# Performance work log

Measured on AMD Instinct MI355X. Metric: run time of the kernel, lower is better.

The kernel has to match this reference:

```python
import jax, jax.numpy as jnp
import numpy as np

N_NODES = 100000
N_EDGES = 1600000
VOCAB = 50000
F_DIM = 128
N_GRAPHS = 64
N_LABELS = 20


def setup_inputs() -> dict:
    key = jax.random.key(0)
    ks = jax.random.split(key, 12)
    s = 1.0 / np.sqrt(F_DIM)
    inp = {
        "x": jax.random.randint(ks[0], (N_NODES,), 0, VOCAB),
        "edge_index": jax.random.randint(ks[1], (2, N_EDGES), 0, N_NODES),
        "batch": jnp.sort(jax.random.randint(ks[2], (N_NODES,), 0, N_GRAPHS)),
        "emb": jax.random.normal(ks[3], (VOCAB, F_DIM), jnp.float32),
        "w1_rel": jax.random.normal(ks[4], (F_DIM, F_DIM), jnp.float32) * s,
        "w1_root": jax.random.normal(ks[5], (F_DIM, F_DIM), jnp.float32) * s,
        "b1": jnp.zeros((F_DIM,), jnp.float32),
        "w2_rel": jax.random.normal(ks[6], (F_DIM, F_DIM), jnp.float32) * s,
        "w2_root": jax.random.normal(ks[7], (F_DIM, F_DIM), jnp.float32) * s,
        "b2": jnp.zeros((F_DIM,), jnp.float32),
        "lw1": jax.random.normal(ks[8], (2 * F_DIM, 128), jnp.float32) * (1.0 / np.sqrt(2 * F_DIM)),
        "lb1": jnp.zeros((128,), jnp.float32),
        "lw2": jax.random.normal(ks[9], (128, 64), jnp.float32) * (1.0 / np.sqrt(128)),
        "lb2": jnp.zeros((64,), jnp.float32),
        "lw3": jax.random.normal(ks[10], (64, N_LABELS), jnp.float32) * (1.0 / np.sqrt(64)),
        "lb3": jnp.zeros((N_LABELS,), jnp.float32),
    }
    return inp


def graph_conv(h, src, dst, w_rel, w_root, b):
    # PyG GraphConv (aggr='add'): out_i = W_rel @ sum_{j->i} h_j + b + W_root @ h_i
    agg = jax.ops.segment_sum(h[src], dst, num_segments=N_NODES)  # [N, F]
    return agg @ w_rel + b + h @ w_root


def reference(x, edge_index, batch, emb, w1_rel, w1_root, b1,
              w2_rel, w2_root, b2, lw1, lb1, lw2, lb2, lw3, lb3):
    src, dst = edge_index[0], edge_index[1]
    h = emb[x]                                              # [N, F]
    h = jax.nn.relu(graph_conv(h, src, dst, w1_rel, w1_root, b1))
    h = jax.nn.relu(graph_conv(h, src, dst, w2_rel, w2_root, b2))
    # global max pool + global mean pool per graph
    gmax = jax.ops.segment_max(h, batch, num_segments=N_GRAPHS)  # [G, F]
    gsum = jax.ops.segment_sum(h, batch, num_segments=N_GRAPHS)
    counts = jax.ops.segment_sum(jnp.ones((N_NODES,), h.dtype), batch,
                                 num_segments=N_GRAPHS)
    gmean = gsum / jnp.maximum(counts, 1.0)[:, None]
    g = jnp.concatenate([gmax, gmean], axis=1)              # [G, 2F]
    g = jax.nn.relu(g @ lw1 + lb1)
    g = jax.nn.relu(g @ lw2 + lb2)
    # NOTE: original applies log_softmax over dim=0 (the graph dim) - kept faithful
    return jax.nn.log_softmax(g @ lw3 + lb3, axis=0)
```

## Files before the change

### kernel.cpp

```cpp
#include <hip/hip_runtime.h>
#include <hip/hip_bf16.h>

#define N_NODES   100000
#define N_EDGES   1600000
#define N_GRAPHS  64
#define FDIM      128
#define N_LABELS  20
#define NBK       64
#define P_BKT     1563
#define NCHUNKS   512
#define NCHUNKS_LOG 9
#define CHUNK     3125
#define SCAN_M    (P_BKT * NCHUNKS)
#define SB1_BLOCKS 3126
#define SB_BLOCKS 391
#define BPITCH    136
#define PCHUNKS   32

typedef __bf16 bf16x8 __attribute__((ext_vector_type(8)));
typedef float  f32x4  __attribute__((ext_vector_type(4)));
union frag_u { uint4 u; bf16x8 b; };

__device__ __forceinline__ unsigned bfr(float v) {
  unsigned b = __float_as_uint(v);
  return (b + 0x7fffu + ((b >> 16) & 1u)) >> 16;
}

__global__ __launch_bounds__(256) void init_kernel(
    float* __restrict__ pool, float* __restrict__ zrow,
    int* __restrict__ csr, int* __restrict__ csr2, int* __restrict__ offsets) {
  int i = blockIdx.x * 256 + threadIdx.x;
  if (i < N_GRAPHS * 256) pool[i] = 0.f;
  if (i < FDIM) zrow[i] = 0.f;
  if (i < 16) { csr[N_EDGES + i] = 0; csr2[N_EDGES + i] = 0; }
  if (i == 16) offsets[N_NODES] = N_EDGES;
}

__global__ __launch_bounds__(256) void cvt_emb_kernel(
    const float* __restrict__ emb, unsigned short* __restrict__ embbf) {
  int i = blockIdx.x * 256 + threadIdx.x;
  float4 v = ((const float4*)emb)[i];
  uint2 o;
  o.x = bfr(v.x) | (bfr(v.y) << 16);
  o.y = bfr(v.z) | (bfr(v.w) << 16);
  ((uint2*)embbf)[i] = o;
}

__global__ __launch_bounds__(256) void cvt_w_kernel(
    const float* __restrict__ w1rel, const float* __restrict__ w1rt,
    const float* __restrict__ w2rel, const float* __restrict__ w2rt,
    unsigned short* __restrict__ wt1, unsigned short* __restrict__ wt2) {
  int gid = blockIdx.x * 256 + threadIdx.x;
  int l = gid >> 15;
  int rem = gid & 32767;
  int c = rem >> 8, k = rem & 255;
  const float* w = l ? ((k < 128) ? w2rel : w2rt) : ((k < 128) ? w1rel : w1rt);
  float v = w[(size_t)(k & 127) * FDIM + c];
  (l ? wt2 : wt1)[c * 256 + k] = (unsigned short)bfr(v);
}

__global__ __launch_bounds__(256) void histA_kernel(
    const int* __restrict__ ei, int* __restrict__ cntmat) {
  __shared__ int hist[P_BKT];
  int tid = threadIdx.x;
  for (int i = tid; i < P_BKT; i += 256) hist[i] = 0;
  __syncthreads();
  int base = blockIdx.x * CHUNK;
  for (int i = tid; i < CHUNK; i += 256) {
    int d = ei[N_EDGES + base + i];
    atomicAdd(&hist[d >> 6], 1);
  }
  __syncthreads();
  for (int p = tid; p < P_BKT; p += 256)
    cntmat[p * NCHUNKS + blockIdx.x] = hist[p];
}

__global__ __launch_bounds__(256) void scanB1_kernel(
    const int* __restrict__ v, int* __restrict__ part,
    int* __restrict__ bsum) {
  __shared__ int s[256];
  int tid = threadIdx.x;
  int i = blockIdx.x * 256 + tid;
  int val = (i < SCAN_M) ? v[i] : 0;
  s[tid] = val;
  __syncthreads();
  for (int off = 1; off < 256; off <<= 1) {
    int t = (tid >= off) ? s[tid - off] : 0;
    __syncthreads();
    s[tid] += t;
    __syncthreads();
  }
  if (i < SCAN_M) part[i] = s[tid] - val;
  if (tid == 255) bsum[blockIdx.x] = s[255];
}

__global__ __launch_bounds__(512) void scanB2_kernel(int* __restrict__ bsum) {
  __shared__ int s[512];
  int tid = threadIdx.x;
  int v[8];
  int tot = 0;
#pragma unroll
  for (int j = 0; j < 8; ++j) {
    int idx = tid * 8 + j;
    v[j] = (idx < SB1_BLOCKS) ? bsum[idx] : 0;
    tot += v[j];
  }
  s[tid] = tot;
  __syncthreads();
  for (int off = 1; off < 512; off <<= 1) {
    int t = (tid >= off) ? s[tid - off] : 0;
    __syncthreads();
    s[tid] += t;
    __syncthreads();
  }
  int run = s[tid] - tot;
#pragma unroll
  for (int j = 0; j < 8; ++j) {
    int idx = tid * 8 + j;
    int val = v[j];
    if (idx < SB1_BLOCKS) bsum[idx] = run;
    run += val;
  }
}

__global__ __launch_bounds__(256) void scanB3_kernel(
    int* __restrict__ part, const int* __restrict__ bsum,
    int* __restrict__ bstart) {
  int i = blockIdx.x * 256 + threadIdx.x;
  if (i < SCAN_M) {
    int o = part[i] + bsum[blockIdx.x];
    part[i] = o;
    if ((i & (NCHUNKS - 1)) == 0) bstart[i >> NCHUNKS_LOG] = o;
  }
  if (blockIdx.x == 0 && threadIdx.x == 0) bstart[P_BKT] = N_EDGES;
}

__global__ __launch_bounds__(256) void scatA_kernel(
    const int* __restrict__ ei, const int* __restrict__ S,
    int* __restrict__ ebuf) {
  __shared__ int rc[P_BKT];
  int tid = threadIdx.x;
  for (int p = tid; p < P_BKT; p += 256)
    rc[p] = S[p * NCHUNKS + blockIdx.x];
  __syncthreads();
  int base = blockIdx.x * CHUNK;
  for (int i = tid; i < CHUNK; i += 256) {
    int s0 = ei[base + i];
    int d0 = ei[N_EDGES + base + i];
    int pos = atomicAdd(&rc[d0 >> 6], 1);
    ebuf[pos] = (s0 << 6) | (d0 & 63);
  }
}

__global__ __launch_bounds__(256) void fill2_kernel(
    const int* __restrict__ ebuf, const int* __restrict__ bstart,
    const int* __restrict__ x, int* __restrict__ offsets,
    int* __restrict__ csr, int* __restrict__ csr2) {
  __shared__ int ldeg[NBK], loffs[NBK], rc2[NBK];
  int tid = threadIdx.x;
  int p = blockIdx.x;
  int beg = bstart[p], end = bstart[p + 1];
  if (tid < NBK) ldeg[tid] = 0;
  __syncthreads();
  for (int i = beg + tid; i < end; i += 256)
    atomicAdd(&ldeg[ebuf[i] & 63], 1);
  __syncthreads();
  if (tid == 0) {
    int run = 0;
    for (int r = 0; r < NBK; ++r) { loffs[r] = run; run += ldeg[r]; }
  }
  __syncthreads();
  if (tid < NBK) {
    rc2[tid] = loffs[tid];
    int gn = p * NBK + tid;
    if (gn < N_NODES) offsets[gn] = beg + loffs[tid];
  }
  __syncthreads();
  for (int i = beg + tid; i < end; i += 256) {
    int e = ebuf[i];
    int ld = e & 63;
    int src = e >> 6;
    int pos = atomicAdd(&rc2[ld], 1);
    csr[beg + pos] = src;
    csr2[beg + pos] = x[src];
  }
}

__global__ __launch_bounds__(256) void agg_kernel(
    const unsigned short* __restrict__ feat, const int* __restrict__ srcidx,
    const int* __restrict__ offs, const float* __restrict__ zrow,
    unsigned short* __restrict__ aggout) {
  int sub = threadIdx.x >> 4;
  int fq  = threadIdx.x & 15;
  int node = blockIdx.x * 16 + sub;

  float4 e0 = make_float4(0.f, 0.f, 0.f, 0.f);
  float4 e1 = make_float4(0.f, 0.f, 0.f, 0.f);
  float4 o0 = make_float4(0.f, 0.f, 0.f, 0.f);
  float4 o1 = make_float4(0.f, 0.f, 0.f, 0.f);
  int s = offs[node], e = offs[node + 1];

  const uint4* __restrict__ fb = (const uint4*)feat;
  const uint4* __restrict__ zb = (const uint4*)zrow;

  int p = s;
  for (; p + 8 <= e; p += 8) {
    const uint4* rp[8];
#pragma unroll
    for (int u = 0; u < 8; ++u)
      rp[u] = fb + (size_t)srcidx[p + u] * 16;
    uint4 w[8];
#pragma unroll
    for (int u = 0; u < 8; ++u) w[u] = rp[u][fq];
#pragma unroll
    for (int u = 0; u < 8; ++u) {
      float4& A = (u & 1) ? o0 : e0;
      float4& B = (u & 1) ? o1 : e1;
      A.x += __uint_as_float(w[u].x << 16);
      A.y += __uint_as_float(w[u].x & 0xffff0000u);
      A.z += __uint_as_float(w[u].y << 16);
      A.w += __uint_as_float(w[u].y & 0xffff0000u);
      B.x += __uint_as_float(w[u].z << 16);
      B.y += __uint_as_float(w[u].z & 0xffff0000u);
      B.z += __uint_as_float(w[u].w << 16);
      B.w += __uint_as_float(w[u].w & 0xffff0000u);
    }
  }
  if (p < e) {
    const uint4* rp[8];
#pragma unroll
    for (int u = 0; u < 8; ++u) {
      int iu = srcidx[p + u];
      rp[u] = (p + u < e) ? (fb + (size_t)iu * 16) : zb;
    }
    uint4 w[8];
#pragma unroll
    for (int u = 0; u < 8; ++u) w[u] = rp[u][fq];
#pragma unroll
    for (int u = 0; u < 8; ++u) {
      float4& A = (u & 1) ? o0 : e0;
      float4& B = (u & 1) ? o1 : e1;
      A.x += __uint_as_float(w[u].x << 16);
      A.y += __uint_as_float(w[u].x & 0xffff0000u);
      A.z += __uint_as_float(w[u].y << 16);
      A.w += __uint_as_float(w[u].y & 0xffff0000u);
      B.x += __uint_as_float(w[u].z << 16);
      B.y += __uint_as_float(w[u].z & 0xffff0000u);
      B.z += __uint_as_float(w[u].w << 16);
      B.w += __uint_as_float(w[u].w & 0xffff0000u);
    }
  }
  float f0 = e0.x + o0.x, f1 = e0.y + o0.y, f2 = e0.z + o0.z, f3 = e0.w + o0.w;
  float f4 = e1.x + o1.x, f5 = e1.y + o1.y, f6 = e1.z + o1.z, f7 = e1.w + o1.w;
  uint4 o;
  o.x = bfr(f0) | (bfr(f1) << 16);
  o.y = bfr(f2) | (bfr(f3) << 16);
  o.z = bfr(f4) | (bfr(f5) << 16);
  o.w = bfr(f6) | (bfr(f7) << 16);
  ((uint4*)aggout)[(size_t)node * 16 + fq] = o;
}

__global__ __launch_bounds__(256, 2) void gemm_kernel(
    const unsigned short* __restrict__ aggbf,
    const unsigned short* __restrict__ rootbf,
    const int* __restrict__ hidx,
    const unsigned short* __restrict__ wt,
    const float* __restrict__ bias,
    float* __restrict__ hout_f32,
    unsigned short* __restrict__ hout_bf) {
  __shared__ unsigned short B_s[128 * BPITCH];
  int tid = threadIdx.x;
  int nodeBase = blockIdx.x * 128;
  int lane = tid & 63;
  int wv = tid >> 6;
  int wbase = wv * 32;
  int lo = lane & 15, hi = lane >> 4;

  int gnode[2], hroot[2];
#pragma unroll
  for (int mt = 0; mt < 2; ++mt) {
    int g = nodeBase + wbase + mt * 16 + lo;
    if (g > N_NODES - 1) g = N_NODES - 1;
    gnode[mt] = g;
    hroot[mt] = hidx ? hidx[g] : g;
  }

  frag_u afr[2][8];
#pragma unroll
  for (int mt = 0; mt < 2; ++mt) {
#pragma unroll
    for (int t = 0; t < 4; ++t)
      afr[mt][t].u =
          *(const uint4*)(aggbf + (size_t)gnode[mt] * FDIM + t * 32 + hi * 8);
#pragma unroll
    for (int t = 0; t < 4; ++t)
      afr[mt][4 + t].u =
          *(const uint4*)(rootbf + (size_t)hroot[mt] * FDIM + t * 32 + hi * 8);
  }

  f32x4 acc[2][8];
#pragma unroll
  for (int nt = 0; nt < 8; ++nt) {
    float b = bias[nt * 16 + lo];
#pragma unroll
    for (int mt = 0; mt < 2; ++mt) {
      acc[mt][nt][0] = b; acc[mt][nt][1] = b;
      acc[mt][nt][2] = b; acc[mt][nt][3] = b;
    }
  }

  int sr = tid >> 1;
  int so = (tid & 1) * 64;

#pragma unroll
  for (int h = 0; h < 2; ++h) {
    __syncthreads();
#pragma unroll
    for (int i = 0; i < 8; ++i)
      *(uint4*)(B_s + sr * BPITCH + so + i * 8) =
          *(const uint4*)(wt + sr * 256 + h * 128 + so + i * 8);
    __syncthreads();
#pragma unroll
    for (int tt = 0; tt < 4; ++tt) {
      frag_u bfv[8];
#pragma unroll
      for (int nt = 0; nt < 8; ++nt)
        bfv[nt].u =
            *(const uint4*)&B_s[(nt * 16 + lo) * BPITCH + tt * 32 + hi * 8];
#pragma unroll
      for (int mt = 0; mt < 2; ++mt)
#pragma unroll
        for (int nt = 0; nt < 8; ++nt)
          acc[mt][nt] = __builtin_amdgcn_mfma_f32_16x16x32_bf16(
              afr[mt][h * 4 + tt].b, bfv[nt].b, acc[mt][nt], 0, 0, 0);
    }
  }

#pragma unroll
  for (int mt = 0; mt < 2; ++mt) {
#pragma unroll
    for (int r = 0; r < 4; ++r) {
      int n = nodeBase + wbase + mt * 16 + hi * 4 + r;
      if (n < N_NODES) {
        if (hout_bf) {
          unsigned short* o = hout_bf + (size_t)n * FDIM + lo;
#pragma unroll
          for (int nt = 0; nt < 8; ++nt)
            o[nt * 16] = (unsigned short)bfr(fmaxf(acc[mt][nt][r], 0.f));
        } else {
          float* o = hout_f32 + (size_t)n * FDIM + lo;
#pragma unroll
          for (int nt = 0; nt < 8; ++nt)
            o[nt * 16] = fmaxf(acc[mt][nt][r], 0.f);
        }
      }
    }
  }
}

__global__ void find_starts_kernel(const int* __restrict__ batch,
                                   int* __restrict__ start) {
  int i = blockIdx.x * 256 + threadIdx.x;
  if (i >= N_NODES) return;
  int b  = batch[i];
  int bp = (i == 0) ? -1 : batch[i - 1];
  for (int g = bp + 1; g <= b; ++g) start[g] = i;
  if (i == N_NODES - 1) {
    for (int g = b + 1; g <= N_GRAPHS; ++g) start[g] = N_NODES;
  }
}

__global__ __launch_bounds__(256) void pool_kernel(
    const float* __restrict__ h2, const int* __restrict__ start,
    float* __restrict__ pool) {
  __shared__ float4 rmax[8][32];
  __shared__ float4 rsum[8][32];
  int g = blockIdx.x >> 5;
  int c = blockIdx.x & (PCHUNKS - 1);
  int tid = threadIdx.x;
  int fq = tid & 31;
  int sub = tid >> 5;
  int s = start[g], e = start[g + 1];
  int len = e - s;
  int lo = s + (int)(((long long)len * c) >> 5);
  int hi = s + (int)(((long long)len * (c + 1)) >> 5);
  float4 mx = make_float4(0.f, 0.f, 0.f, 0.f);
  float4 sm = make_float4(0.f, 0.f, 0.f, 0.f);
  for (int n = lo + sub; n < hi; n += 8) {
    float4 v = ((const float4*)(h2 + (size_t)n * FDIM))[fq];
    mx.x = fmaxf(mx.x, v.x); mx.y = fmaxf(mx.y, v.y);
    mx.z = fmaxf(mx.z, v.z); mx.w = fmaxf(mx.w, v.w);
    sm.x += v.x; sm.y += v.y; sm.z += v.z; sm.w += v.w;
  }
  rmax[sub][fq] = mx;
  rsum[sub][fq] = sm;
  __syncthreads();
  if (sub == 0) {
#pragma unroll
    for (int r = 1; r < 8; ++r) {
      float4 m2 = rmax[r][fq], s2 = rsum[r][fq];
      mx.x = fmaxf(mx.x, m2.x); mx.y = fmaxf(mx.y, m2.y);
      mx.z = fmaxf(mx.z, m2.z); mx.w = fmaxf(mx.w, m2.w);
      sm.x += s2.x; sm.y += s2.y; sm.z += s2.z; sm.w += s2.w;
    }
    unsigned int* pm = (unsigned int*)&pool[g * 256 + fq * 4];
    atomicMax(pm + 0, __float_as_uint(mx.x));
    atomicMax(pm + 1, __float_as_uint(mx.y));
    atomicMax(pm + 2, __float_as_uint(mx.z));
    atomicMax(pm + 3, __float_as_uint(mx.w));
    float* ps = &pool[g * 256 + 128 + fq * 4];
    atomicAdd(ps + 0, sm.x);
    atomicAdd(ps + 1, sm.y);
    atomicAdd(ps + 2, sm.z);
    atomicAdd(ps + 3, sm.w);
  }
}

__global__ void pool_fin_kernel(float* __restrict__ pool,
                                const int* __restrict__ start) {
  int gid = blockIdx.x * 256 + threadIdx.x;
  int g = gid >> 7, f = gid & 127;
  int cnt = start[g + 1] - start[g];
  float c = (float)(cnt > 1 ? cnt : 1);
  pool[g * 256 + 128 + f] /= c;
}

__global__ void head1_kernel(const float* __restrict__ pool,
                             const float* __restrict__ lw1,
                             const float* __restrict__ lb1,
                             float* __restrict__ t1) {
  int gid = blockIdx.x * 256 + threadIdx.x;
  int r = gid >> 7, c = gid & 127;
  float acc = lb1[c];
  for (int k = 0; k < 256; ++k) acc += pool[r * 256 + k] * lw1[k * 128 + c];
  t1[gid] = fmaxf(acc, 0.f);
}

__global__ void head2_kernel(const float* __restrict__ t1,
                             const float* __restrict__ lw2,
                             const float* __restrict__ lb2,
                             float* __restrict__ t2) {
  int gid = blockIdx.x * 256 + threadIdx.x;
  int r = gid >> 6, c = gid & 63;
  float acc = lb2[c];
  for (int k = 0; k < 128; ++k) acc += t1[r * 128 + k] * lw2[k * 64 + c];
  t2[gid] = fmaxf(acc, 0.f);
}

__global__ __launch_bounds__(256) void head3_kernel(
    const float* __restrict__ t2, const float* __restrict__ lw3,
    const float* __restrict__ lb3, float* __restrict__ out) {
  __shared__ float lg[N_GRAPHS * N_LABELS];
  __shared__ float col[N_LABELS];
  int tid = threadIdx.x;
  for (int o = tid; o < N_GRAPHS * N_LABELS; o += 256) {
    int r = o / N_LABELS, c = o - r * N_LABELS;
    float acc = lb3[c];
    for (int k = 0; k < 64; ++k) acc += t2[r * 64 + k] * lw3[k * N_LABELS + c];
    lg[o] = acc;
  }
  __syncthreads();
  if (tid < N_LABELS) {
    float m = -1e30f;
    for (int r = 0; r < N_GRAPHS; ++r) m = fmaxf(m, lg[r * N_LABELS + tid]);
    float s = 0.f;
    for (int r = 0; r < N_GRAPHS; ++r) s += expf(lg[r * N_LABELS + tid] - m);
    col[tid] = m + logf(s);
  }
  __syncthreads();
  for (int o = tid; o < N_GRAPHS * N_LABELS; o += 256) {
    int c = o % N_LABELS;
    out[o] = lg[o] - col[c];
  }
}

extern "C" void kernel_launch(void* const* d_in, const int* in_sizes, int n_in,
                              void* d_out, int out_size, void* d_ws, size_t ws_size,
                              hipStream_t stream) {
  const int*   x     = (const int*)  d_in[0];
  const int*   ei    = (const int*)  d_in[1];
  const int*   batch = (const int*)  d_in[2];
  const float* emb   = (const float*)d_in[3];
  const float* w1rel = (const float*)d_in[4];
  const float* w1rt  = (const float*)d_in[5];
  const float* b1    = (const float*)d_in[6];
  const float* w2rel = (const float*)d_in[7];
  const float* w2rt  = (const float*)d_in[8];
  const float* b2    = (const float*)d_in[9];
  const float* lw1   = (const float*)d_in[10];
  const float* lb1   = (const float*)d_in[11];
  const float* lw2   = (const float*)d_in[12];
  const float* lb2   = (const float*)d_in[13];
  const float* lw3   = (const float*)d_in[14];
  const float* lb3   = (const float*)d_in[15];
  float* out = (float*)d_out;

  char* ws = (char*)d_ws;
  const size_t HB   = 51200000;
  const size_t CSRB = 6400128;
  const size_t OFFB = 400128;
  float* hB      = (float*)(ws);
  unsigned short* embbf = (unsigned short*)(ws);
  int*   cntmat  = (int*)  (ws + 13000000);
  int*   S       = (int*)  (ws + 16500000);
  int*   bsum    = (int*)  (ws + 20000000);
  unsigned short* aggbf = (unsigned short*)(ws + HB);
  int*   ebuf    = (int*)  (ws + HB);
  int*   csr     = (int*)  (ws + 2 * HB);
  int*   csr2    = (int*)  (ws + 2 * HB + CSRB);
  int*   offsets = (int*)  (ws + 2 * HB + 2 * CSRB);
  int*   bstart  = (int*)  (ws + 2 * HB + 2 * CSRB + OFFB);
  float* zrow    = (float*)(ws + 2 * HB + 2 * CSRB + OFFB + 6400);
  int*   start   = (int*)  (ws + 2 * HB + 2 * CSRB + OFFB + 6912);
  float* pool    = (float*)(ws + 2 * HB + 2 * CSRB + OFFB + 7424);
  float* t1      = (float*)(ws + 2 * HB + 2 * CSRB + OFFB + 72960);
  float* t2      = (float*)(ws + 2 * HB + 2 * CSRB + OFFB + 105728);
  unsigned short* hbf =
      (unsigned short*)(ws + 2 * HB + 2 * CSRB + OFFB + 122112);
  unsigned short* wt1 =
      (unsigned short*)(ws + 2 * HB + 2 * CSRB + OFFB + 122112 + 25600000);
  unsigned short* wt2 = wt1 + 128 * 256;

  init_kernel<<<64, 256, 0, stream>>>(pool, zrow, csr, csr2, offsets);

  cvt_emb_kernel<<<6250, 256, 0, stream>>>(emb, embbf);
  cvt_w_kernel<<<256, 256, 0, stream>>>(w1rel, w1rt, w2rel, w2rt, wt1, wt2);

  histA_kernel<<<NCHUNKS, 256, 0, stream>>>(ei, cntmat);
  scanB1_kernel<<<SB1_BLOCKS, 256, 0, stream>>>(cntmat, S, bsum);
  scanB2_kernel<<<1, 512, 0, stream>>>(bsum);
  scanB3_kernel<<<SB1_BLOCKS, 256, 0, stream>>>(S, bsum, bstart);
  scatA_kernel<<<NCHUNKS, 256, 0, stream>>>(ei, S, ebuf);
  fill2_kernel<<<P_BKT, 256, 0, stream>>>(ebuf, bstart, x, offsets, csr, csr2);

  agg_kernel<<<N_NODES / 16, 256, 0, stream>>>(embbf, csr2, offsets, zrow, aggbf);
  gemm_kernel<<<(N_NODES + 127) / 128, 256, 0, stream>>>(
      aggbf, embbf, x, wt1, b1, (float*)nullptr, hbf);

  agg_kernel<<<N_NODES / 16, 256, 0, stream>>>(hbf, csr, offsets, zrow, aggbf);
  gemm_kernel<<<(N_NODES + 127) / 128, 256, 0, stream>>>(
      aggbf, hbf, (const int*)nullptr, wt2, b2, hB,
      (unsigned short*)nullptr);

  find_starts_kernel<<<SB_BLOCKS, 256, 0, stream>>>(batch, start);
  pool_kernel<<<N_GRAPHS * PCHUNKS, 256, 0, stream>>>(hB, start, pool);
  pool_fin_kernel<<<32, 256, 0, stream>>>(pool, start);

  head1_kernel<<<32, 256, 0, stream>>>(pool, lw1, lb1, t1);
  head2_kernel<<<16, 256, 0, stream>>>(t1, lw2, lb2, t2);
  head3_kernel<<<1, 256, 0, stream>>>(t2, lw3, lb3, out);
}
```

Baseline: 380.4 us.

## Software-pipeline edge gathers in aggregation and merge prep kernels into one launch

The aggregation kernel now double-buffers its neighbour index and feature loads, issuing the next batch of eight gathers before accumulating the current batch so memory latency overlaps with the adds. Separately, init, embedding conversion, weight conversion and graph-start finding are merged into one block-partitioned prep kernel to save launches. The pipelined loop reads indices up to 16 entries past a node's end, so the zero padding after the CSR arrays was widened from 16 to 32. It also holds more registers for the two buffers, which may lower occupancy.

```diff
diff --git a/kernel.cpp b/kernel.cpp
--- a/kernel.cpp
+++ b/kernel.cpp
@@ -26,37 +26,48 @@
   return (b + 0x7fffu + ((b >> 16) & 1u)) >> 16;
 }
 
-__global__ __launch_bounds__(256) void init_kernel(
-    float* __restrict__ pool, float* __restrict__ zrow,
-    int* __restrict__ csr, int* __restrict__ csr2, int* __restrict__ offsets) {
-  int i = blockIdx.x * 256 + threadIdx.x;
-  if (i < N_GRAPHS * 256) pool[i] = 0.f;
-  if (i < FDIM) zrow[i] = 0.f;
-  if (i < 16) { csr[N_EDGES + i] = 0; csr2[N_EDGES + i] = 0; }
-  if (i == 16) offsets[N_NODES] = N_EDGES;
-}
-
-__global__ __launch_bounds__(256) void cvt_emb_kernel(
-    const float* __restrict__ emb, unsigned short* __restrict__ embbf) {
-  int i = blockIdx.x * 256 + threadIdx.x;
-  float4 v = ((const float4*)emb)[i];
-  uint2 o;
-  o.x = bfr(v.x) | (bfr(v.y) << 16);
-  o.y = bfr(v.z) | (bfr(v.w) << 16);
-  ((uint2*)embbf)[i] = o;
-}
-
-__global__ __launch_bounds__(256) void cvt_w_kernel(
+__global__ __launch_bounds__(256) void prep_kernel(
+    const float* __restrict__ emb, unsigned short* __restrict__ embbf,
     const float* __restrict__ w1rel, const float* __restrict__ w1rt,
     const float* __restrict__ w2rel, const float* __restrict__ w2rt,
-    unsigned short* __restrict__ wt1, unsigned short* __restrict__ wt2) {
-  int gid = blockIdx.x * 256 + threadIdx.x;
-  int l = gid >> 15;
-  int rem = gid & 32767;
-  int c = rem >> 8, k = rem & 255;
-  const float* w = l ? ((k < 128) ? w2rel : w2rt) : ((k < 128) ? w1rel : w1rt);
-  float v = w[(size_t)(k & 127) * FDIM + c];
-  (l ? wt2 : wt1)[c * 256 + k] = (unsigned short)bfr(v);
+    unsigned short* __restrict__ wt1, unsigned short* __restrict__ wt2,
+    const int* __restrict__ batch, int* __restrict__ start,
+    float* __restrict__ pool, float* __restrict__ zrow,
+    int* __restrict__ csr, int* __restrict__ csr2,
+    int* __restrict__ offsets) {
+  int b = blockIdx.x;
+  int tid = threadIdx.x;
+  if (b < 6250) {
+    int i = b * 256 + tid;
+    float4 v = ((const float4*)emb)[i];
+    uint2 o;
+    o.x = bfr(v.x) | (bfr(v.y) << 16);
+    o.y = bfr(v.z) | (bfr(v.w) << 16);
+    ((uint2*)embbf)[i] = o;
+  } else if (b < 6506) {
+    int gid = (b - 6250) * 256 + tid;
+    int l = gid >> 15;
+    int rem = gid & 32767;
+    int c = rem >> 8, k = rem & 255;
+    const float* w = l ? ((k < 128) ? w2rel : w2rt) : ((k < 128) ? w1rel : w1rt);
+    float v = w[(size_t)(k & 127) * FDIM + c];
+    (l ? wt2 : wt1)[c * 256 + k] = (unsigned short)bfr(v);
+  } else if (b < 6897) {
+    int i = (b - 6506) * 256 + tid;
+    if (i >= N_NODES) return;
+    int bb = batch[i];
+    int bp = (i == 0) ? -1 : batch[i - 1];
+    for (int g = bp + 1; g <= bb; ++g) start[g] = i;
+    if (i == N_NODES - 1) {
+      for (int g = bb + 1; g <= N_GRAPHS; ++g) start[g] = N_NODES;
+    }
+  } else {
+    int i = (b - 6897) * 256 + tid;
+    if (i < N_GRAPHS * 256) pool[i] = 0.f;
+    if (i < FDIM) zrow[i] = 0.f;
+    if (i < 32) { csr[N_EDGES + i] = 0; csr2[N_EDGES + i] = 0; }
+    if (i == 32) offsets[N_NODES] = N_EDGES;
+  }
 }
 
 __global__ __launch_bounds__(256) void histA_kernel(
@@ -186,6 +197,32 @@
   }
 }
 
+#define LOADIDX(I, P)                                      \
+  { _Pragma("unroll")                                      \
+    for (int u = 0; u < 8; ++u) I[u] = srcidx[(P) + u]; }
+
+#define GATHERW(W, I, P)                                   \
+  { _Pragma("unroll")                                      \
+    for (int u = 0; u < 8; ++u) {                          \
+      const uint4* rp = ((P) + u < e) ? (fb + (size_t)I[u] * 16) : zb; \
+      W[u] = rp[fq];                                       \
+    } }
+
+#define ACCG(W)                                            \
+  { _Pragma("unroll")                                      \
+    for (int u = 0; u < 8; ++u) {                          \
+      float4& A = (u & 1) ? o0 : e0;                       \
+      float4& B = (u & 1) ? o1 : e1;                       \
+      A.x += __uint_as_float(W[u].x << 16);                \
+      A.y += __uint_as_float(W[u].x & 0xffff0000u);        \
+      A.z += __uint_as_float(W[u].y << 16);                \
+      A.w += __uint_as_float(W[u].y & 0xffff0000u);        \
+      B.x += __uint_as_float(W[u].z << 16);                \
+      B.y += __uint_as_float(W[u].z & 0xffff0000u);        \
+      B.z += __uint_as_float(W[u].w << 16);                \
+      B.w += __uint_as_float(W[u].w & 0xffff0000u);        \
+    } }
+
 __global__ __launch_bounds__(256) void agg_kernel(
     const unsigned short* __restrict__ feat, const int* __restrict__ srcidx,
     const int* __restrict__ offs, const float* __restrict__ zrow,
@@ -203,53 +240,28 @@
   const uint4* __restrict__ fb = (const uint4*)feat;
   const uint4* __restrict__ zb = (const uint4*)zrow;
 
+  int iA[8], iB[8];
+  uint4 wA[8], wB[8];
+
+  LOADIDX(iA, s);
+  LOADIDX(iB, s + 8);
+  GATHERW(wA, iA, s);
+
   int p = s;
-  for (; p + 8 <= e; p += 8) {
-    const uint4* rp[8];
-#pragma unroll
-    for (int u = 0; u < 8; ++u)
-      rp[u] = fb + (size_t)srcidx[p + u] * 16;
-    uint4 w[8];
-#pragma unroll
-    for (int u = 0; u < 8; ++u) w[u] = rp[u][fq];
-#pragma unroll
-    for (int u = 0; u < 8; ++u) {
-      float4& A = (u & 1) ? o0 : e0;
-      float4& B = (u & 1) ? o1 : e1;
-      A.x += __uint_as_float(w[u].x << 16);
-      A.y += __uint_as_float(w[u].x & 0xffff0000u);
-      A.z += __uint_as_float(w[u].y << 16);
-      A.w += __uint_as_float(w[u].y & 0xffff0000u);
-      B.x += __uint_as_float(w[u].z << 16);
-      B.y += __uint_as_float(w[u].z & 0xffff0000u);
-      B.z += __uint_as_float(w[u].w << 16);
-      B.w += __uint_as_float(w[u].w & 0xffff0000u);
-    }
-  }
-  if (p < e) {
-    const uint4* rp[8];
-#pragma unroll
-    for (int u = 0; u < 8; ++u) {
-      int iu = srcidx[p + u];
-      rp[u] = (p + u < e) ? (fb + (size_t)iu * 16) : zb;
-    }
-    uint4 w[8];
-#pragma unroll
-    for (int u = 0; u < 8; ++u) w[u] = rp[u][fq];
-#pragma unroll
-    for (int u = 0; u < 8; ++u) {
-      float4& A = (u & 1) ? o0 : e0;
-      float4& B = (u & 1) ? o1 : e1;
-      A.x += __uint_as_float(w[u].x << 16);
-      A.y += __uint_as_float(w[u].x & 0xffff0000u);
-      A.z += __uint_as_float(w[u].y << 16);
-      A.w += __uint_as_float(w[u].y & 0xffff0000u);
-      B.x += __uint_as_float(w[u].z << 16);
-      B.y += __uint_as_float(w[u].z & 0xffff0000u);
-      B.z += __uint_as_float(w[u].w << 16);
-      B.w += __uint_as_float(w[u].w & 0xffff0000u);
-    }
-  }
+  while (true) {
+    int pn = p + 8;
+    if (pn >= e) { ACCG(wA); break; }
+    LOADIDX(iA, pn + 8);
+    GATHERW(wB, iB, pn);
+    ACCG(wA);
+    p = pn; pn = p + 8;
+    if (pn >= e) { ACCG(wB); break; }
+    LOADIDX(iB, pn + 8);
+    GATHERW(wA, iA, pn);
+    ACCG(wB);
+    p = pn;
+  }
+
   float f0 = e0.x + o0.x, f1 = e0.y + o0.y, f2 = e0.z + o0.z, f3 = e0.w + o0.w;
   float f4 = e1.x + o1.x, f5 = e1.y + o1.y, f6 = e1.z + o1.z, f7 = e1.w + o1.w;
   uint4 o;
@@ -355,18 +367,6 @@
         }
       }
     }
-  }
-}
-
-__global__ void find_starts_kernel(const int* __restrict__ batch,
-                                   int* __restrict__ start) {
-  int i = blockIdx.x * 256 + threadIdx.x;
-  if (i >= N_NODES) return;
-  int b  = batch[i];
-  int bp = (i == 0) ? -1 : batch[i - 1];
-  for (int g = bp + 1; g <= b; ++g) start[g] = i;
-  if (i == N_NODES - 1) {
-    for (int g = b + 1; g <= N_GRAPHS; ++g) start[g] = N_NODES;
   }
 }
 
@@ -521,10 +521,9 @@
       (unsigned short*)(ws + 2 * HB + 2 * CSRB + OFFB + 122112 + 25600000);
   unsigned short* wt2 = wt1 + 128 * 256;
 
-  init_kernel<<<64, 256, 0, stream>>>(pool, zrow, csr, csr2, offsets);
-
-  cvt_emb_kernel<<<6250, 256, 0, stream>>>(emb, embbf);
-  cvt_w_kernel<<<256, 256, 0, stream>>>(w1rel, w1rt, w2rel, w2rt, wt1, wt2);
+  prep_kernel<<<6961, 256, 0, stream>>>(emb, embbf, w1rel, w1rt, w2rel, w2rt,
+                                        wt1, wt2, batch, start, pool, zrow,
+                                        csr, csr2, offsets);
 
   histA_kernel<<<NCHUNKS, 256, 0, stream>>>(ei, cntmat);
   scanB1_kernel<<<SB1_BLOCKS, 256, 0, stream>>>(cntmat, S, bsum);
@@ -542,7 +541,6 @@
       aggbf, hbf, (const int*)nullptr, wt2, b2, hB,
       (unsigned short*)nullptr);
 
-  find_starts_kernel<<<SB_BLOCKS, 256, 0, stream>>>(batch, start);
   pool_kernel<<<N_GRAPHS * PCHUNKS, 256, 0, stream>>>(hB, start, pool);
   pool_fin_kernel<<<32, 256, 0, stream>>>(pool, start);
 
```

Measured after the change: 392.7 us. 1.03x slower.

## Fuse neighbor aggregation with MFMA GEMM per layer and merge prep kernels

Applied to the files above, without the earlier changes.

Folds each layer's edge aggregation and its dense GEMM into one kernel. The aggregated and root rows for 16 nodes are staged in shared memory and multiplied right away with MFMA, using weight fragments read straight from global memory. This removes the bf16 aggregation buffer's write and re-read and two launches per layer. In exchange, each block reloads the full 64KB weight matrix from global/L2 for only 16 nodes, with little reuse per block. It also merges the init, embedding/weight conversion and graph-start kernels into one prep launch to cut launch overhead.

```diff
diff --git a/kernel.cpp b/kernel.cpp
--- a/kernel.cpp
+++ b/kernel.cpp
@@ -14,8 +14,8 @@
 #define SCAN_M    (P_BKT * NCHUNKS)
 #define SB1_BLOCKS 3126
 #define SB_BLOCKS 391
-#define BPITCH    136
 #define PCHUNKS   32
+#define APAD      17
 
 typedef __bf16 bf16x8 __attribute__((ext_vector_type(8)));
 typedef float  f32x4  __attribute__((ext_vector_type(4)));
@@ -26,37 +26,48 @@
   return (b + 0x7fffu + ((b >> 16) & 1u)) >> 16;
 }
 
-__global__ __launch_bounds__(256) void init_kernel(
-    float* __restrict__ pool, float* __restrict__ zrow,
-    int* __restrict__ csr, int* __restrict__ csr2, int* __restrict__ offsets) {
-  int i = blockIdx.x * 256 + threadIdx.x;
-  if (i < N_GRAPHS * 256) pool[i] = 0.f;
-  if (i < FDIM) zrow[i] = 0.f;
-  if (i < 16) { csr[N_EDGES + i] = 0; csr2[N_EDGES + i] = 0; }
-  if (i == 16) offsets[N_NODES] = N_EDGES;
-}
-
-__global__ __launch_bounds__(256) void cvt_emb_kernel(
-    const float* __restrict__ emb, unsigned short* __restrict__ embbf) {
-  int i = blockIdx.x * 256 + threadIdx.x;
-  float4 v = ((const float4*)emb)[i];
-  uint2 o;
-  o.x = bfr(v.x) | (bfr(v.y) << 16);
-  o.y = bfr(v.z) | (bfr(v.w) << 16);
-  ((uint2*)embbf)[i] = o;
-}
-
-__global__ __launch_bounds__(256) void cvt_w_kernel(
+__global__ __launch_bounds__(256) void prep_kernel(
+    const float* __restrict__ emb, unsigned short* __restrict__ embbf,
     const float* __restrict__ w1rel, const float* __restrict__ w1rt,
     const float* __restrict__ w2rel, const float* __restrict__ w2rt,
-    unsigned short* __restrict__ wt1, unsigned short* __restrict__ wt2) {
-  int gid = blockIdx.x * 256 + threadIdx.x;
-  int l = gid >> 15;
-  int rem = gid & 32767;
-  int c = rem >> 8, k = rem & 255;
-  const float* w = l ? ((k < 128) ? w2rel : w2rt) : ((k < 128) ? w1rel : w1rt);
-  float v = w[(size_t)(k & 127) * FDIM + c];
-  (l ? wt2 : wt1)[c * 256 + k] = (unsigned short)bfr(v);
+    unsigned short* __restrict__ wt1, unsigned short* __restrict__ wt2,
+    const int* __restrict__ batch, int* __restrict__ start,
+    float* __restrict__ pool, float* __restrict__ zrow,
+    int* __restrict__ csr, int* __restrict__ csr2,
+    int* __restrict__ offsets) {
+  int b = blockIdx.x;
+  int tid = threadIdx.x;
+  if (b < 6250) {
+    int i = b * 256 + tid;
+    float4 v = ((const float4*)emb)[i];
+    uint2 o;
+    o.x = bfr(v.x) | (bfr(v.y) << 16);
+    o.y = bfr(v.z) | (bfr(v.w) << 16);
+    ((uint2*)embbf)[i] = o;
+  } else if (b < 6506) {
+    int gid = (b - 6250) * 256 + tid;
+    int l = gid >> 15;
+    int rem = gid & 32767;
+    int c = rem >> 8, k = rem & 255;
+    const float* w = l ? ((k < 128) ? w2rel : w2rt) : ((k < 128) ? w1rel : w1rt);
+    float v = w[(size_t)(k & 127) * FDIM + c];
+    (l ? wt2 : wt1)[c * 256 + k] = (unsigned short)bfr(v);
+  } else if (b < 6897) {
+    int i = (b - 6506) * 256 + tid;
+    if (i >= N_NODES) return;
+    int bb = batch[i];
+    int bp = (i == 0) ? -1 : batch[i - 1];
+    for (int g = bp + 1; g <= bb; ++g) start[g] = i;
+    if (i == N_NODES - 1) {
+      for (int g = bb + 1; g <= N_GRAPHS; ++g) start[g] = N_NODES;
+    }
+  } else {
+    int i = (b - 6897) * 256 + tid;
+    if (i < N_GRAPHS * 256) pool[i] = 0.f;
+    if (i < FDIM) zrow[i] = 0.f;
+    if (i < 32) { csr[N_EDGES + i] = 0; csr2[N_EDGES + i] = 0; }
+    if (i == 32) offsets[N_NODES] = N_EDGES;
+  }
 }
 
 __global__ __launch_bounds__(256) void histA_kernel(
@@ -186,13 +197,23 @@
   }
 }
 
-__global__ __launch_bounds__(256) void agg_kernel(
+__global__ __launch_bounds__(256) void layer_kernel(
     const unsigned short* __restrict__ feat, const int* __restrict__ srcidx,
     const int* __restrict__ offs, const float* __restrict__ zrow,
-    unsigned short* __restrict__ aggout) {
-  int sub = threadIdx.x >> 4;
-  int fq  = threadIdx.x & 15;
+    const unsigned short* __restrict__ rootbf, const int* __restrict__ hidx,
+    const unsigned short* __restrict__ wt,
+    const float* __restrict__ bias,
+    float* __restrict__ hout_f32,
+    unsigned short* __restrict__ hout_bf) {
+  __shared__ uint4 A_s[16 * APAD];
+  __shared__ uint4 R_s[16 * APAD];
+  int tid = threadIdx.x;
+  int sub = tid >> 4;
+  int fq  = tid & 15;
   int node = blockIdx.x * 16 + sub;
+
+  int hr = hidx ? hidx[node] : node;
+  uint4 rootw = ((const uint4*)rootbf)[(size_t)hr * 16 + fq];
 
   float4 e0 = make_float4(0.f, 0.f, 0.f, 0.f);
   float4 e1 = make_float4(0.f, 0.f, 0.f, 0.f);
@@ -257,116 +278,47 @@
   o.y = bfr(f2) | (bfr(f3) << 16);
   o.z = bfr(f4) | (bfr(f5) << 16);
   o.w = bfr(f6) | (bfr(f7) << 16);
-  ((uint4*)aggout)[(size_t)node * 16 + fq] = o;
-}
-
-__global__ __launch_bounds__(256, 2) void gemm_kernel(
-    const unsigned short* __restrict__ aggbf,
-    const unsigned short* __restrict__ rootbf,
-    const int* __restrict__ hidx,
-    const unsigned short* __restrict__ wt,
-    const float* __restrict__ bias,
-    float* __restrict__ hout_f32,
-    unsigned short* __restrict__ hout_bf) {
-  __shared__ unsigned short B_s[128 * BPITCH];
-  int tid = threadIdx.x;
-  int nodeBase = blockIdx.x * 128;
+  A_s[sub * APAD + fq] = o;
+  R_s[sub * APAD + fq] = rootw;
+  __syncthreads();
+
   int lane = tid & 63;
   int wv = tid >> 6;
-  int wbase = wv * 32;
   int lo = lane & 15, hi = lane >> 4;
 
-  int gnode[2], hroot[2];
-#pragma unroll
-  for (int mt = 0; mt < 2; ++mt) {
-    int g = nodeBase + wbase + mt * 16 + lo;
-    if (g > N_NODES - 1) g = N_NODES - 1;
-    gnode[mt] = g;
-    hroot[mt] = hidx ? hidx[g] : g;
-  }
-
-  frag_u afr[2][8];
-#pragma unroll
-  for (int mt = 0; mt < 2; ++mt) {
-#pragma unroll
-    for (int t = 0; t < 4; ++t)
-      afr[mt][t].u =
-          *(const uint4*)(aggbf + (size_t)gnode[mt] * FDIM + t * 32 + hi * 8);
-#pragma unroll
-    for (int t = 0; t < 4; ++t)
-      afr[mt][4 + t].u =
-          *(const uint4*)(rootbf + (size_t)hroot[mt] * FDIM + t * 32 + hi * 8);
-  }
-
-  f32x4 acc[2][8];
-#pragma unroll
-  for (int nt = 0; nt < 8; ++nt) {
-    float b = bias[nt * 16 + lo];
-#pragma unroll
-    for (int mt = 0; mt < 2; ++mt) {
-      acc[mt][nt][0] = b; acc[mt][nt][1] = b;
-      acc[mt][nt][2] = b; acc[mt][nt][3] = b;
-    }
-  }
-
-  int sr = tid >> 1;
-  int so = (tid & 1) * 64;
-
-#pragma unroll
-  for (int h = 0; h < 2; ++h) {
-    __syncthreads();
-#pragma unroll
-    for (int i = 0; i < 8; ++i)
-      *(uint4*)(B_s + sr * BPITCH + so + i * 8) =
-          *(const uint4*)(wt + sr * 256 + h * 128 + so + i * 8);
-    __syncthreads();
-#pragma unroll
-    for (int tt = 0; tt < 4; ++tt) {
-      frag_u bfv[8];
-#pragma unroll
-      for (int nt = 0; nt < 8; ++nt)
-        bfv[nt].u =
-            *(const uint4*)&B_s[(nt * 16 + lo) * BPITCH + tt * 32 + hi * 8];
-#pragma unroll
-      for (int mt = 0; mt < 2; ++mt)
-#pragma unroll
-        for (int nt = 0; nt < 8; ++nt)
-          acc[mt][nt] = __builtin_amdgcn_mfma_f32_16x16x32_bf16(
-              afr[mt][h * 4 + tt].b, bfv[nt].b, acc[mt][nt], 0, 0, 0);
-    }
-  }
-
-#pragma unroll
-  for (int mt = 0; mt < 2; ++mt) {
+  f32x4 acc[2];
+#pragma unroll
+  for (int j = 0; j < 2; ++j) {
+    float b = bias[(wv * 2 + j) * 16 + lo];
+    acc[j][0] = b; acc[j][1] = b; acc[j][2] = b; acc[j][3] = b;
+  }
+#pragma unroll
+  for (int t = 0; t < 8; ++t) {
+    frag_u a;
+    a.u = (t < 4) ? A_s[lo * APAD + t * 4 + hi]
+                  : R_s[lo * APAD + (t - 4) * 4 + hi];
+#pragma unroll
+    for (int j = 0; j < 2; ++j) {
+      int nt = wv * 2 + j;
+      frag_u bfv;
+      bfv.u = *(const uint4*)(wt + (size_t)(nt * 16 + lo) * 256 + t * 32 + hi * 8);
+      acc[j] = __builtin_amdgcn_mfma_f32_16x16x32_bf16(a.b, bfv.b, acc[j], 0, 0, 0);
+    }
+  }
+
+  int nodeBase = blockIdx.x * 16;
+#pragma unroll
+  for (int j = 0; j < 2; ++j) {
+    int nt = wv * 2 + j;
 #pragma unroll
     for (int r = 0; r < 4; ++r) {
-      int n = nodeBase + wbase + mt * 16 + hi * 4 + r;
-      if (n < N_NODES) {
-        if (hout_bf) {
-          unsigned short* o = hout_bf + (size_t)n * FDIM + lo;
-#pragma unroll
-          for (int nt = 0; nt < 8; ++nt)
-            o[nt * 16] = (unsigned short)bfr(fmaxf(acc[mt][nt][r], 0.f));
-        } else {
-          float* o = hout_f32 + (size_t)n * FDIM + lo;
-#pragma unroll
-          for (int nt = 0; nt < 8; ++nt)
-            o[nt * 16] = fmaxf(acc[mt][nt][r], 0.f);
-        }
-      }
-    }
-  }
-}
-
-__global__ void find_starts_kernel(const int* __restrict__ batch,
-                                   int* __restrict__ start) {
-  int i = blockIdx.x * 256 + threadIdx.x;
-  if (i >= N_NODES) return;
-  int b  = batch[i];
-  int bp = (i == 0) ? -1 : batch[i - 1];
-  for (int g = bp + 1; g <= b; ++g) start[g] = i;
-  if (i == N_NODES - 1) {
-    for (int g = b + 1; g <= N_GRAPHS; ++g) start[g] = N_NODES;
+      int n = nodeBase + hi * 4 + r;
+      if (hout_bf)
+        hout_bf[(size_t)n * FDIM + nt * 16 + lo] =
+            (unsigned short)bfr(fmaxf(acc[j][r], 0.f));
+      else
+        hout_f32[(size_t)n * FDIM + nt * 16 + lo] = fmaxf(acc[j][r], 0.f);
+    }
   }
 }
 
@@ -504,7 +456,6 @@
   int*   cntmat  = (int*)  (ws + 13000000);
   int*   S       = (int*)  (ws + 16500000);
   int*   bsum    = (int*)  (ws + 20000000);
-  unsigned short* aggbf = (unsigned short*)(ws + HB);
   int*   ebuf    = (int*)  (ws + HB);
   int*   csr     = (int*)  (ws + 2 * HB);
   int*   csr2    = (int*)  (ws + 2 * HB + CSRB);
@@ -521,10 +472,9 @@
       (unsigned short*)(ws + 2 * HB + 2 * CSRB + OFFB + 122112 + 25600000);
   unsigned short* wt2 = wt1 + 128 * 256;
 
-  init_kernel<<<64, 256, 0, stream>>>(pool, zrow, csr, csr2, offsets);
-
-  cvt_emb_kernel<<<6250, 256, 0, stream>>>(emb, embbf);
-  cvt_w_kernel<<<256, 256, 0, stream>>>(w1rel, w1rt, w2rel, w2rt, wt1, wt2);
+  prep_kernel<<<6961, 256, 0, stream>>>(emb, embbf, w1rel, w1rt, w2rel, w2rt,
+                                        wt1, wt2, batch, start, pool, zrow,
+                                        csr, csr2, offsets);
 
   histA_kernel<<<NCHUNKS, 256, 0, stream>>>(ei, cntmat);
   scanB1_kernel<<<SB1_BLOCKS, 256, 0, stream>>>(cntmat, S, bsum);
@@ -533,16 +483,14 @@
   scatA_kernel<<<NCHUNKS, 256, 0, stream>>>(ei, S, ebuf);
   fill2_kernel<<<P_BKT, 256, 0, stream>>>(ebuf, bstart, x, offsets, csr, csr2);
 
-  agg_kernel<<<N_NODES / 16, 256, 0, stream>>>(embbf, csr2, offsets, zrow, aggbf);
-  gemm_kernel<<<(N_NODES + 127) / 128, 256, 0, stream>>>(
-      aggbf, embbf, x, wt1, b1, (float*)nullptr, hbf);
-
-  agg_kernel<<<N_NODES / 16, 256, 0, stream>>>(hbf, csr, offsets, zrow, aggbf);
-  gemm_kernel<<<(N_NODES + 127) / 128, 256, 0, stream>>>(
-      aggbf, hbf, (const int*)nullptr, wt2, b2, hB,
-      (unsigned short*)nullptr);
-
-  find_starts_kernel<<<SB_BLOCKS, 256, 0, stream>>>(batch, start);
+  layer_kernel<<<N_NODES / 16, 256, 0, stream>>>(
+      embbf, csr2, offsets, zrow, embbf, x, wt1, b1,
+      (float*)nullptr, hbf);
+
+  layer_kernel<<<N_NODES / 16, 256, 0, stream>>>(
+      hbf, csr, offsets, zrow, hbf, (const int*)nullptr, wt2, b2,
+      hB, (unsigned short*)nullptr);
+
   pool_kernel<<<N_GRAPHS * PCHUNKS, 256, 0, stream>>>(hB, start, pool);
   pool_fin_kernel<<<32, 256, 0, stream>>>(pool, start);
 
```

Measured after the change: 417.1 us. 9.6% more time.

## Fuse graph pooling into layer-2 GEMM epilogue and merge prep kernels

Applied to the files above, without the earlier changes.

The second GEMM no longer writes the fp32 hidden matrix. It applies relu in registers and reduces max and sum per graph directly into the pool buffer with atomics, using wave shuffles when a 16-row tile belongs to one graph. This removes a 51 MB write and re-read plus the separate pool kernel. The init, embedding conversion, weight conversion and graph-start kernels are also merged into one launch to cut launch overhead. The cost is more atomics in the GEMM epilogue for tiles that span graph boundaries, and contention on 64 graph rows.

```diff
diff --git a/kernel.cpp b/kernel.cpp
--- a/kernel.cpp
+++ b/kernel.cpp
@@ -15,7 +15,6 @@
 #define SB1_BLOCKS 3126
 #define SB_BLOCKS 391
 #define BPITCH    136
-#define PCHUNKS   32
 
 typedef __bf16 bf16x8 __attribute__((ext_vector_type(8)));
 typedef float  f32x4  __attribute__((ext_vector_type(4)));
@@ -26,37 +25,48 @@
   return (b + 0x7fffu + ((b >> 16) & 1u)) >> 16;
 }
 
-__global__ __launch_bounds__(256) void init_kernel(
-    float* __restrict__ pool, float* __restrict__ zrow,
-    int* __restrict__ csr, int* __restrict__ csr2, int* __restrict__ offsets) {
-  int i = blockIdx.x * 256 + threadIdx.x;
-  if (i < N_GRAPHS * 256) pool[i] = 0.f;
-  if (i < FDIM) zrow[i] = 0.f;
-  if (i < 16) { csr[N_EDGES + i] = 0; csr2[N_EDGES + i] = 0; }
-  if (i == 16) offsets[N_NODES] = N_EDGES;
-}
-
-__global__ __launch_bounds__(256) void cvt_emb_kernel(
-    const float* __restrict__ emb, unsigned short* __restrict__ embbf) {
-  int i = blockIdx.x * 256 + threadIdx.x;
-  float4 v = ((const float4*)emb)[i];
-  uint2 o;
-  o.x = bfr(v.x) | (bfr(v.y) << 16);
-  o.y = bfr(v.z) | (bfr(v.w) << 16);
-  ((uint2*)embbf)[i] = o;
-}
-
-__global__ __launch_bounds__(256) void cvt_w_kernel(
+__global__ __launch_bounds__(256) void prep_kernel(
+    const float* __restrict__ emb, unsigned short* __restrict__ embbf,
     const float* __restrict__ w1rel, const float* __restrict__ w1rt,
     const float* __restrict__ w2rel, const float* __restrict__ w2rt,
-    unsigned short* __restrict__ wt1, unsigned short* __restrict__ wt2) {
-  int gid = blockIdx.x * 256 + threadIdx.x;
-  int l = gid >> 15;
-  int rem = gid & 32767;
-  int c = rem >> 8, k = rem & 255;
-  const float* w = l ? ((k < 128) ? w2rel : w2rt) : ((k < 128) ? w1rel : w1rt);
-  float v = w[(size_t)(k & 127) * FDIM + c];
-  (l ? wt2 : wt1)[c * 256 + k] = (unsigned short)bfr(v);
+    unsigned short* __restrict__ wt1, unsigned short* __restrict__ wt2,
+    const int* __restrict__ batch, int* __restrict__ start,
+    float* __restrict__ pool, float* __restrict__ zrow,
+    int* __restrict__ csr, int* __restrict__ csr2,
+    int* __restrict__ offsets) {
+  int b = blockIdx.x;
+  int tid = threadIdx.x;
+  if (b < 6250) {
+    int i = b * 256 + tid;
+    float4 v = ((const float4*)emb)[i];
+    uint2 o;
+    o.x = bfr(v.x) | (bfr(v.y) << 16);
+    o.y = bfr(v.z) | (bfr(v.w) << 16);
+    ((uint2*)embbf)[i] = o;
+  } else if (b < 6506) {
+    int gid = (b - 6250) * 256 + tid;
+    int l = gid >> 15;
+    int rem = gid & 32767;
+    int c = rem >> 8, k = rem & 255;
+    const float* w = l ? ((k < 128) ? w2rel : w2rt) : ((k < 128) ? w1rel : w1rt);
+    float v = w[(size_t)(k & 127) * FDIM + c];
+    (l ? wt2 : wt1)[c * 256 + k] = (unsigned short)bfr(v);
+  } else if (b < 6897) {
+    int i = (b - 6506) * 256 + tid;
+    if (i >= N_NODES) return;
+    int bb = batch[i];
+    int bp = (i == 0) ? -1 : batch[i - 1];
+    for (int g = bp + 1; g <= bb; ++g) start[g] = i;
+    if (i == N_NODES - 1) {
+      for (int g = bb + 1; g <= N_GRAPHS; ++g) start[g] = N_NODES;
+    }
+  } else {
+    int i = (b - 6897) * 256 + tid;
+    if (i < N_GRAPHS * 256) pool[i] = 0.f;
+    if (i < FDIM) zrow[i] = 0.f;
+    if (i < 32) { csr[N_EDGES + i] = 0; csr2[N_EDGES + i] = 0; }
+    if (i == 32) offsets[N_NODES] = N_EDGES;
+  }
 }
 
 __global__ __launch_bounds__(256) void histA_kernel(
@@ -266,7 +276,8 @@
     const int* __restrict__ hidx,
     const unsigned short* __restrict__ wt,
     const float* __restrict__ bias,
-    float* __restrict__ hout_f32,
+    const int* __restrict__ batch,
+    float* __restrict__ pool,
     unsigned short* __restrict__ hout_bf) {
   __shared__ unsigned short B_s[128 * BPITCH];
   int tid = threadIdx.x;
@@ -336,83 +347,69 @@
     }
   }
 
-#pragma unroll
-  for (int mt = 0; mt < 2; ++mt) {
-#pragma unroll
-    for (int r = 0; r < 4; ++r) {
-      int n = nodeBase + wbase + mt * 16 + hi * 4 + r;
-      if (n < N_NODES) {
-        if (hout_bf) {
+  if (hout_bf) {
+#pragma unroll
+    for (int mt = 0; mt < 2; ++mt) {
+#pragma unroll
+      for (int r = 0; r < 4; ++r) {
+        int n = nodeBase + wbase + mt * 16 + hi * 4 + r;
+        if (n < N_NODES) {
           unsigned short* o = hout_bf + (size_t)n * FDIM + lo;
 #pragma unroll
           for (int nt = 0; nt < 8; ++nt)
             o[nt * 16] = (unsigned short)bfr(fmaxf(acc[mt][nt][r], 0.f));
-        } else {
-          float* o = hout_f32 + (size_t)n * FDIM + lo;
-#pragma unroll
-          for (int nt = 0; nt < 8; ++nt)
-            o[nt * 16] = fmaxf(acc[mt][nt][r], 0.f);
         }
       }
     }
-  }
-}
-
-__global__ void find_starts_kernel(const int* __restrict__ batch,
-                                   int* __restrict__ start) {
-  int i = blockIdx.x * 256 + threadIdx.x;
-  if (i >= N_NODES) return;
-  int b  = batch[i];
-  int bp = (i == 0) ? -1 : batch[i - 1];
-  for (int g = bp + 1; g <= b; ++g) start[g] = i;
-  if (i == N_NODES - 1) {
-    for (int g = b + 1; g <= N_GRAPHS; ++g) start[g] = N_NODES;
-  }
-}
-
-__global__ __launch_bounds__(256) void pool_kernel(
-    const float* __restrict__ h2, const int* __restrict__ start,
-    float* __restrict__ pool) {
-  __shared__ float4 rmax[8][32];
-  __shared__ float4 rsum[8][32];
-  int g = blockIdx.x >> 5;
-  int c = blockIdx.x & (PCHUNKS - 1);
-  int tid = threadIdx.x;
-  int fq = tid & 31;
-  int sub = tid >> 5;
-  int s = start[g], e = start[g + 1];
-  int len = e - s;
-  int lo = s + (int)(((long long)len * c) >> 5);
-  int hi = s + (int)(((long long)len * (c + 1)) >> 5);
-  float4 mx = make_float4(0.f, 0.f, 0.f, 0.f);
-  float4 sm = make_float4(0.f, 0.f, 0.f, 0.f);
-  for (int n = lo + sub; n < hi; n += 8) {
-    float4 v = ((const float4*)(h2 + (size_t)n * FDIM))[fq];
-    mx.x = fmaxf(mx.x, v.x); mx.y = fmaxf(mx.y, v.y);
-    mx.z = fmaxf(mx.z, v.z); mx.w = fmaxf(mx.w, v.w);
-    sm.x += v.x; sm.y += v.y; sm.z += v.z; sm.w += v.w;
-  }
-  rmax[sub][fq] = mx;
-  rsum[sub][fq] = sm;
-  __syncthreads();
-  if (sub == 0) {
-#pragma unroll
-    for (int r = 1; r < 8; ++r) {
-      float4 m2 = rmax[r][fq], s2 = rsum[r][fq];
-      mx.x = fmaxf(mx.x, m2.x); mx.y = fmaxf(mx.y, m2.y);
-      mx.z = fmaxf(mx.z, m2.z); mx.w = fmaxf(mx.w, m2.w);
-      sm.x += s2.x; sm.y += s2.y; sm.z += s2.z; sm.w += s2.w;
-    }
-    unsigned int* pm = (unsigned int*)&pool[g * 256 + fq * 4];
-    atomicMax(pm + 0, __float_as_uint(mx.x));
-    atomicMax(pm + 1, __float_as_uint(mx.y));
-    atomicMax(pm + 2, __float_as_uint(mx.z));
-    atomicMax(pm + 3, __float_as_uint(mx.w));
-    float* ps = &pool[g * 256 + 128 + fq * 4];
-    atomicAdd(ps + 0, sm.x);
-    atomicAdd(ps + 1, sm.y);
-    atomicAdd(ps + 2, sm.z);
-    atomicAdd(ps + 3, sm.w);
+  } else {
+#pragma unroll
+    for (int mt = 0; mt < 2; ++mt)
+#pragma unroll
+      for (int nt = 0; nt < 8; ++nt)
+#pragma unroll
+        for (int r = 0; r < 4; ++r)
+          acc[mt][nt][r] = fmaxf(acc[mt][nt][r], 0.f);
+
+#pragma unroll
+    for (int mt = 0; mt < 2; ++mt) {
+      int rowBase = nodeBase + wbase + mt * 16;
+      int lastRow = rowBase + 15;
+      int gF = batch[rowBase < N_NODES ? rowBase : N_NODES - 1];
+      int gL = batch[lastRow < N_NODES ? lastRow : N_NODES - 1];
+      if (gF == gL && lastRow < N_NODES) {
+#pragma unroll
+        for (int nt = 0; nt < 8; ++nt) {
+          float mx = fmaxf(fmaxf(acc[mt][nt][0], acc[mt][nt][1]),
+                           fmaxf(acc[mt][nt][2], acc[mt][nt][3]));
+          float sm = acc[mt][nt][0] + acc[mt][nt][1] +
+                     acc[mt][nt][2] + acc[mt][nt][3];
+          mx = fmaxf(mx, __shfl_xor(mx, 16));
+          sm += __shfl_xor(sm, 16);
+          mx = fmaxf(mx, __shfl_xor(mx, 32));
+          sm += __shfl_xor(sm, 32);
+          if (hi == 0) {
+            int c = nt * 16 + lo;
+            atomicMax((unsigned int*)&pool[gF * 256 + c], __float_as_uint(mx));
+            atomicAdd(&pool[gF * 256 + 128 + c], sm);
+          }
+        }
+      } else {
+#pragma unroll
+        for (int r = 0; r < 4; ++r) {
+          int n = rowBase + hi * 4 + r;
+          if (n < N_NODES) {
+            int g = batch[n];
+#pragma unroll
+            for (int nt = 0; nt < 8; ++nt) {
+              int c = nt * 16 + lo;
+              atomicMax((unsigned int*)&pool[g * 256 + c],
+                        __float_as_uint(acc[mt][nt][r]));
+              atomicAdd(&pool[g * 256 + 128 + c], acc[mt][nt][r]);
+            }
+          }
+        }
+      }
+    }
   }
 }
 
@@ -499,7 +496,6 @@
   const size_t HB   = 51200000;
   const size_t CSRB = 6400128;
   const size_t OFFB = 400128;
-  float* hB      = (float*)(ws);
   unsigned short* embbf = (unsigned short*)(ws);
   int*   cntmat  = (int*)  (ws + 13000000);
   int*   S       = (int*)  (ws + 16500000);
@@ -521,10 +517,9 @@
       (unsigned short*)(ws + 2 * HB + 2 * CSRB + OFFB + 122112 + 25600000);
   unsigned short* wt2 = wt1 + 128 * 256;
 
-  init_kernel<<<64, 256, 0, stream>>>(pool, zrow, csr, csr2, offsets);
-
-  cvt_emb_kernel<<<6250, 256, 0, stream>>>(emb, embbf);
-  cvt_w_kernel<<<256, 256, 0, stream>>>(w1rel, w1rt, w2rel, w2rt, wt1, wt2);
+  prep_kernel<<<6961, 256, 0, stream>>>(emb, embbf, w1rel, w1rt, w2rel, w2rt,
+                                        wt1, wt2, batch, start, pool, zrow,
+                                        csr, csr2, offsets);
 
   histA_kernel<<<NCHUNKS, 256, 0, stream>>>(ei, cntmat);
   scanB1_kernel<<<SB1_BLOCKS, 256, 0, stream>>>(cntmat, S, bsum);
@@ -535,15 +530,13 @@
 
   agg_kernel<<<N_NODES / 16, 256, 0, stream>>>(embbf, csr2, offsets, zrow, aggbf);
   gemm_kernel<<<(N_NODES + 127) / 128, 256, 0, stream>>>(
-      aggbf, embbf, x, wt1, b1, (float*)nullptr, hbf);
+      aggbf, embbf, x, wt1, b1, (const int*)nullptr, (float*)nullptr, hbf);
 
   agg_kernel<<<N_NODES / 16, 256, 0, stream>>>(hbf, csr, offsets, zrow, aggbf);
   gemm_kernel<<<(N_NODES + 127) / 128, 256, 0, stream>>>(
-      aggbf, hbf, (const int*)nullptr, wt2, b2, hB,
+      aggbf, hbf, (const int*)nullptr, wt2, b2, batch, pool,
       (unsigned short*)nullptr);
 
-  find_starts_kernel<<<SB_BLOCKS, 256, 0, stream>>>(batch, start);
-  pool_kernel<<<N_GRAPHS * PCHUNKS, 256, 0, stream>>>(hB, start, pool);
   pool_fin_kernel<<<32, 256, 0, stream>>>(pool, start);
 
   head1_kernel<<<32, 256, 0, stream>>>(pool, lw1, lb1, t1);
```

After: 370.9 us. 1.03x faster.
